# Kernel tuning notes

Measured on AMD Instinct MI355X. Metric: run time of the kernel, lower is better.

## Reference

```python
import jax, jax.numpy as jnp
import numpy as np

B, S, N, C, OUT = 16, 1024, 4096, 768, 256


def setup_inputs() -> dict:
    key = jax.random.key(0)
    k0, k1, k2, k3, k4 = jax.random.split(key, 5)
    seed_xyz = jax.random.normal(k0, (B, S, 3), jnp.float32)   # normalized seed coords
    p_last = jax.random.normal(k1, (B, N, 3), jnp.float32)     # lift3d last-stage coords
    f_last = jax.random.normal(k2, (B, C, N), jnp.float32)     # lift3d last-stage features (channel-first)
    W = jax.random.normal(k3, (OUT, C), jnp.float32) * 0.02    # Conv1d(C, 256, kernel_size=1) weight
    b = jax.random.normal(k4, (OUT,), jnp.float32) * 0.02      # Conv1d bias
    return {"seed_xyz": seed_xyz, "p_last": p_last, "f_last": f_last, "W": W, "b": b}


def reference(seed_xyz, p_last, f_last, W, b):
    # Squared pairwise distances [B,S,N] (argmin invariant to sqrt)
    d2 = (jnp.sum(seed_xyz * seed_xyz, axis=-1, keepdims=True)          # [B,S,1]
          - 2.0 * jnp.einsum('bsd,bnd->bsn', seed_xyz, p_last)          # [B,S,N]
          + jnp.sum(p_last * p_last, axis=-1)[:, None, :])              # [B,1,N]
    idx = jnp.argmin(d2, axis=-1)                                       # [B,S]
    # Gather nearest-neighbor features: [B,C,N] -> [B,C,S]
    gathered = jnp.take_along_axis(f_last, idx[:, None, :], axis=2)
    # 1x1 Conv1d projector: [B,C,S] x [OUT,C] -> [B,OUT,S]
    seed_features = jnp.einsum('bcs,oc->bos', gathered, W) + b[None, :, None]
    return seed_features
```

## Files before the change

kernel.cpp:

```cpp
#include <hip/hip_runtime.h>
#include <stdint.h>

#define B_   16
#define S_   1024
#define N_   4096
#define C_   768
#define OUT_ 256

typedef short bf16x8 __attribute__((ext_vector_type(8)));
typedef short bf16x4 __attribute__((ext_vector_type(4)));
typedef float f32x4  __attribute__((ext_vector_type(4)));

#define GLOBAL_AS __attribute__((address_space(1)))
#define LDS_AS    __attribute__((address_space(3)))

__device__ __forceinline__ unsigned short f2bf(float f) {
    unsigned int u = __float_as_uint(f);
    u += 0x7fffu + ((u >> 16) & 1u);
    return (unsigned short)(u >> 16);
}

__device__ __forceinline__ void gl_lds16(const void* gsrc, void* ldst) {
    __builtin_amdgcn_global_load_lds((const GLOBAL_AS void*)gsrc,
                                     (LDS_AS void*)ldst, 16, 0, 0);
}

__global__ __launch_bounds__(256) void k_wconv(const float* __restrict__ W,
                                               unsigned short* __restrict__ Wb) {
    int i = blockIdx.x * 256 + threadIdx.x;
    Wb[i] = f2bf(W[i]);
}

__global__ __launch_bounds__(256) void k_argmin(const float* __restrict__ seed,
                                                const float* __restrict__ pl,
                                                int* __restrict__ idx_out) {
    const int t    = threadIdx.x;
    const int lane = t & 63;
    const int w    = t >> 6;
    const int gw   = blockIdx.x * 4 + w;
    const int b    = gw >> 8;
    const int s0   = (gw & 255) * 4;

    float sx[4], sy[4], sz[4], s2[4], best[4];
    int   bidx[4];
#pragma unroll
    for (int j = 0; j < 4; ++j) {
        const float* sp = seed + (size_t)(b * S_ + s0 + j) * 3;
        sx[j] = sp[0]; sy[j] = sp[1]; sz[j] = sp[2];
        s2[j] = __fadd_rn(__fadd_rn(__fmul_rn(sx[j], sx[j]),
                                    __fmul_rn(sy[j], sy[j])),
                          __fmul_rn(sz[j], sz[j]));
        best[j] = 3.4e38f;
        bidx[j] = 0;
    }
    const float* pb = pl + (size_t)b * N_ * 3;

    for (int k = 0; k < N_ / 64; ++k) {
        const int   n  = k * 64 + lane;
        const float px = pb[n * 3 + 0];
        const float py = pb[n * 3 + 1];
        const float pz = pb[n * 3 + 2];
        const float p2 = __fadd_rn(__fadd_rn(__fmul_rn(px, px),
                                             __fmul_rn(py, py)),
                                   __fmul_rn(pz, pz));
#pragma unroll
        for (int j = 0; j < 4; ++j) {
            float dot = __fadd_rn(__fadd_rn(__fmul_rn(sx[j], px),
                                            __fmul_rn(sy[j], py)),
                                  __fmul_rn(sz[j], pz));
            float d2  = __fadd_rn(__fsub_rn(s2[j], __fmul_rn(2.0f, dot)), p2);
            if (d2 < best[j]) { best[j] = d2; bidx[j] = n; }
        }
    }

#pragma unroll
    for (int j = 0; j < 4; ++j) {
#pragma unroll
        for (int off = 32; off >= 1; off >>= 1) {
            float ob = __shfl_xor(best[j], off, 64);
            int   oi = __shfl_xor(bidx[j], off, 64);
            bool take = (ob < best[j]) || (ob == best[j] && oi < bidx[j]);
            if (take) { best[j] = ob; bidx[j] = oi; }
        }
        if (lane == 0) idx_out[b * S_ + s0 + j] = bidx[j];
    }
}

__global__ __launch_bounds__(256, 2) void k_pgemm(const float* __restrict__ f,
                                                  const unsigned short* __restrict__ Wb,
                                                  unsigned short* __restrict__ P) {
    __shared__ unsigned short ldsF[128 * 36];
    __shared__ unsigned short ldsW[256 * 32];
    const int t    = threadIdx.x;
    const int b    = blockIdx.x >> 5;
    const int nt   = blockIdx.x & 31;
    const int n0   = nt * 128;
    const int lane = t & 63;
    const int w    = t >> 6;
    const int wm   = w & 1;
    const int wo   = w >> 1;
    const int quad = lane >> 4, l16 = lane & 15;

    f32x4 acc[4][8];
#pragma unroll
    for (int i = 0; i < 4; ++i)
#pragma unroll
        for (int j = 0; j < 8; ++j) acc[i][j] = (f32x4){0.f, 0.f, 0.f, 0.f};

    const int cb = t >> 5;
    const int nb = t & 31;
    const float* fB = f + (size_t)b * C_ * N_ + n0 + nb * 4;
    const unsigned short* wSrc = Wb + (size_t)(t >> 2) * C_ + (t & 3) * 8;

    for (int kt = 0; kt < C_ / 32; ++kt) {
        const int k0 = kt * 32;
#pragma unroll
        for (int i = 0; i < 4; ++i)
            gl_lds16(wSrc + (size_t)i * 64 * C_ + k0, ldsW + i * 2048 + t * 8);
        f32x4 v[4];
#pragma unroll
        for (int j = 0; j < 4; ++j)
            v[j] = *(const f32x4*)(fB + (size_t)(k0 + cb * 4 + j) * N_);
#pragma unroll
        for (int i = 0; i < 4; ++i) {
            bf16x4 pk = {(short)f2bf(v[0][i]), (short)f2bf(v[1][i]),
                         (short)f2bf(v[2][i]), (short)f2bf(v[3][i])};
            *(bf16x4*)(ldsF + (nb * 4 + i) * 36 + cb * 4) = pk;
        }
        __syncthreads();

        bf16x8 aF[4], bF[8];
#pragma unroll
        for (int mi = 0; mi < 4; ++mi) {
            const unsigned short* p = ldsF + (wm * 64 + mi * 16 + l16) * 36 + quad * 8;
            bf16x4 lo = *(const bf16x4*)p;
            bf16x4 hi = *(const bf16x4*)(p + 4);
            aF[mi] = __builtin_shufflevector(lo, hi, 0, 1, 2, 3, 4, 5, 6, 7);
        }
#pragma unroll
        for (int oi = 0; oi < 8; ++oi)
            bF[oi] = *(const bf16x8*)(ldsW + (wo * 128 + oi * 16 + l16) * 32 + quad * 8);
#pragma unroll
        for (int mi = 0; mi < 4; ++mi)
#pragma unroll
            for (int oi = 0; oi < 8; ++oi)
                acc[mi][oi] = __builtin_amdgcn_mfma_f32_16x16x32_bf16(
                    aF[mi], bF[oi], acc[mi][oi], 0, 0, 0);
        __syncthreads();
    }

    unsigned short* Pb = P + ((size_t)b * N_ + n0) * OUT_;
#pragma unroll
    for (int mi = 0; mi < 4; ++mi) {
#pragma unroll
        for (int r = 0; r < 4; ++r) {
            const int n = wm * 64 + mi * 16 + quad * 4 + r;
            unsigned short* row = Pb + (size_t)n * OUT_;
#pragma unroll
            for (int oi = 0; oi < 8; ++oi) {
                const int o = wo * 128 + oi * 16 + l16;
                row[o] = f2bf(acc[mi][oi][r]);
            }
        }
    }
}

__global__ __launch_bounds__(256) void k_out(const unsigned short* __restrict__ P,
                                             const int* __restrict__ idx,
                                             const float* __restrict__ bias,
                                             float* __restrict__ out) {
    __shared__ unsigned short tl[64 * 260];
    const int t  = threadIdx.x;
    const int b  = blockIdx.x >> 4;
    const int st = blockIdx.x & 15;
    const int s0 = st * 64;
    const unsigned short* Pb = P + (size_t)b * N_ * OUT_;

#pragma unroll
    for (int i = 0; i < 8; ++i) {
        const int g = i * 256 + t;
        const int s = g >> 5;
        const int p = g & 31;
        const int n = idx[b * S_ + s0 + s];
        const unsigned short* src = Pb + (size_t)n * OUT_ + p * 8;
        uint2 u0 = *(const uint2*)src;
        uint2 u1 = *(const uint2*)(src + 4);
        *(uint2*)(tl + s * 260 + p * 8)     = u0;
        *(uint2*)(tl + s * 260 + p * 8 + 4) = u1;
    }
    __syncthreads();

    const int lane = t & 63;
    const int w    = t >> 6;
    float* ob = out + (size_t)b * OUT_ * S_ + s0;
#pragma unroll 4
    for (int oo = 0; oo < 64; ++oo) {
        const int o = w * 64 + oo;
        const unsigned short u = tl[lane * 260 + o];
        const float val = __uint_as_float(((unsigned int)u) << 16) + bias[o];
        ob[(size_t)o * S_ + lane] = val;
    }
}

extern "C" void kernel_launch(void* const* d_in, const int* in_sizes, int n_in,
                              void* d_out, int out_size, void* d_ws, size_t ws_size,
                              hipStream_t stream) {
    const float* seed = (const float*)d_in[0];
    const float* pl   = (const float*)d_in[1];
    const float* f    = (const float*)d_in[2];
    const float* W    = (const float*)d_in[3];
    const float* bias = (const float*)d_in[4];
    float* out = (float*)d_out;

    int* idx            = (int*)d_ws;
    unsigned short* Wb  = (unsigned short*)((char*)d_ws + 65536);
    unsigned short* P   = (unsigned short*)((char*)d_ws + 524288);

    k_wconv <<<768,  256, 0, stream>>>(W, Wb);
    k_argmin<<<1024, 256, 0, stream>>>(seed, pl, idx);
    k_pgemm <<<512,  256, 0, stream>>>(f, Wb, P);
    k_out   <<<256,  256, 0, stream>>>(P, idx, bias, out);
}
```

Before: 320.9 us.

## Fuse argmin into projector GEMM kernel and double-buffer GEMM LDS tiles

Merges the nearest-neighbour argmin and the feature projection GEMM into one launch. Every third block runs argmin over 16 seeds per wave, and the other blocks run the GEMM, so the ALU-bound search can overlap with the memory-bound GEMM on the same device. The GEMM loop now double-buffers its LDS tiles: the next K-slice is loaded while MFMAs run on the current one. The cost is twice the LDS per block, more registers in the argmin path (16 seeds per wave), and fewer argmin blocks, each doing more work, which could leave argmin blocks as stragglers.

```diff
diff --git a/kernel.cpp b/kernel.cpp
--- a/kernel.cpp
+++ b/kernel.cpp
@@ -31,70 +31,72 @@
     Wb[i] = f2bf(W[i]);
 }
 
-__global__ __launch_bounds__(256) void k_argmin(const float* __restrict__ seed,
-                                                const float* __restrict__ pl,
-                                                int* __restrict__ idx_out) {
-    const int t    = threadIdx.x;
-    const int lane = t & 63;
-    const int w    = t >> 6;
-    const int gw   = blockIdx.x * 4 + w;
-    const int b    = gw >> 8;
-    const int s0   = (gw & 255) * 4;
-
-    float sx[4], sy[4], sz[4], s2[4], best[4];
-    int   bidx[4];
-#pragma unroll
-    for (int j = 0; j < 4; ++j) {
-        const float* sp = seed + (size_t)(b * S_ + s0 + j) * 3;
-        sx[j] = sp[0]; sy[j] = sp[1]; sz[j] = sp[2];
-        s2[j] = __fadd_rn(__fadd_rn(__fmul_rn(sx[j], sx[j]),
-                                    __fmul_rn(sy[j], sy[j])),
-                          __fmul_rn(sz[j], sz[j]));
-        best[j] = 3.4e38f;
-        bidx[j] = 0;
-    }
-    const float* pb = pl + (size_t)b * N_ * 3;
-
-    for (int k = 0; k < N_ / 64; ++k) {
-        const int   n  = k * 64 + lane;
-        const float px = pb[n * 3 + 0];
-        const float py = pb[n * 3 + 1];
-        const float pz = pb[n * 3 + 2];
-        const float p2 = __fadd_rn(__fadd_rn(__fmul_rn(px, px),
-                                             __fmul_rn(py, py)),
-                                   __fmul_rn(pz, pz));
-#pragma unroll
-        for (int j = 0; j < 4; ++j) {
-            float dot = __fadd_rn(__fadd_rn(__fmul_rn(sx[j], px),
-                                            __fmul_rn(sy[j], py)),
-                                  __fmul_rn(sz[j], pz));
-            float d2  = __fadd_rn(__fsub_rn(s2[j], __fmul_rn(2.0f, dot)), p2);
-            if (d2 < best[j]) { best[j] = d2; bidx[j] = n; }
-        }
-    }
-
-#pragma unroll
-    for (int j = 0; j < 4; ++j) {
-#pragma unroll
-        for (int off = 32; off >= 1; off >>= 1) {
-            float ob = __shfl_xor(best[j], off, 64);
-            int   oi = __shfl_xor(bidx[j], off, 64);
-            bool take = (ob < best[j]) || (ob == best[j] && oi < bidx[j]);
-            if (take) { best[j] = ob; bidx[j] = oi; }
-        }
-        if (lane == 0) idx_out[b * S_ + s0 + j] = bidx[j];
-    }
-}
-
-__global__ __launch_bounds__(256, 2) void k_pgemm(const float* __restrict__ f,
+__global__ __launch_bounds__(256, 2) void k_fused(const float* __restrict__ f,
                                                   const unsigned short* __restrict__ Wb,
-                                                  unsigned short* __restrict__ P) {
-    __shared__ unsigned short ldsF[128 * 36];
-    __shared__ unsigned short ldsW[256 * 32];
-    const int t    = threadIdx.x;
-    const int b    = blockIdx.x >> 5;
-    const int nt   = blockIdx.x & 31;
-    const int n0   = nt * 128;
+                                                  const float* __restrict__ seed,
+                                                  const float* __restrict__ pl,
+                                                  unsigned short* __restrict__ P,
+                                                  int* __restrict__ idx_out) {
+    __shared__ unsigned short ldsF[2][128 * 36];
+    __shared__ unsigned short ldsW[2][256 * 32];
+    const int t   = threadIdx.x;
+    const int bid = blockIdx.x;
+    const int q   = bid / 3;
+    const int r   = bid - q * 3;
+
+    if (r == 2) {
+        const int lane = t & 63;
+        const int w    = t >> 6;
+        const int b    = q >> 4;
+        const int s0   = (q & 15) * 64 + w * 16;
+
+        float sx[16], sy[16], sz[16], s2[16], best[16];
+        int   bidx[16];
+#pragma unroll
+        for (int j = 0; j < 16; ++j) {
+            const float* sp = seed + (size_t)(b * S_ + s0 + j) * 3;
+            sx[j] = sp[0]; sy[j] = sp[1]; sz[j] = sp[2];
+            s2[j] = __fadd_rn(__fadd_rn(__fmul_rn(sx[j], sx[j]),
+                                        __fmul_rn(sy[j], sy[j])),
+                              __fmul_rn(sz[j], sz[j]));
+            best[j] = 3.4e38f;
+            bidx[j] = 0;
+        }
+        const float* pb = pl + (size_t)b * N_ * 3;
+        for (int k = 0; k < N_ / 64; ++k) {
+            const int   n  = k * 64 + lane;
+            const float px = pb[n * 3 + 0];
+            const float py = pb[n * 3 + 1];
+            const float pz = pb[n * 3 + 2];
+            const float p2 = __fadd_rn(__fadd_rn(__fmul_rn(px, px),
+                                                 __fmul_rn(py, py)),
+                                       __fmul_rn(pz, pz));
+#pragma unroll
+            for (int j = 0; j < 16; ++j) {
+                float dot = __fadd_rn(__fadd_rn(__fmul_rn(sx[j], px),
+                                                __fmul_rn(sy[j], py)),
+                                      __fmul_rn(sz[j], pz));
+                float d2  = __fadd_rn(__fsub_rn(s2[j], __fmul_rn(2.0f, dot)), p2);
+                if (d2 < best[j]) { best[j] = d2; bidx[j] = n; }
+            }
+        }
+#pragma unroll
+        for (int j = 0; j < 16; ++j) {
+#pragma unroll
+            for (int off = 32; off >= 1; off >>= 1) {
+                float ob = __shfl_xor(best[j], off, 64);
+                int   oi = __shfl_xor(bidx[j], off, 64);
+                bool take = (ob < best[j]) || (ob == best[j] && oi < bidx[j]);
+                if (take) { best[j] = ob; bidx[j] = oi; }
+            }
+            if (lane == 0) idx_out[b * S_ + s0 + j] = bidx[j];
+        }
+        return;
+    }
+
+    const int pid  = q * 2 + r;
+    const int b    = pid >> 5;
+    const int n0   = (pid & 31) * 128;
     const int lane = t & 63;
     const int w    = t >> 6;
     const int wm   = w & 1;
@@ -112,40 +114,60 @@
     const float* fB = f + (size_t)b * C_ * N_ + n0 + nb * 4;
     const unsigned short* wSrc = Wb + (size_t)(t >> 2) * C_ + (t & 3) * 8;
 
-    for (int kt = 0; kt < C_ / 32; ++kt) {
-        const int k0 = kt * 32;
-#pragma unroll
-        for (int i = 0; i < 4; ++i)
-            gl_lds16(wSrc + (size_t)i * 64 * C_ + k0, ldsW + i * 2048 + t * 8);
-        f32x4 v[4];
-#pragma unroll
-        for (int j = 0; j < 4; ++j)
-            v[j] = *(const f32x4*)(fB + (size_t)(k0 + cb * 4 + j) * N_);
-#pragma unroll
-        for (int i = 0; i < 4; ++i) {
-            bf16x4 pk = {(short)f2bf(v[0][i]), (short)f2bf(v[1][i]),
-                         (short)f2bf(v[2][i]), (short)f2bf(v[3][i])};
-            *(bf16x4*)(ldsF + (nb * 4 + i) * 36 + cb * 4) = pk;
-        }
-        __syncthreads();
+    f32x4 v[4];
+#pragma unroll
+    for (int i = 0; i < 4; ++i)
+        gl_lds16(wSrc + (size_t)i * 64 * C_, &ldsW[0][i * 2048 + t * 8]);
+#pragma unroll
+    for (int j = 0; j < 4; ++j)
+        v[j] = *(const f32x4*)(fB + (size_t)(cb * 4 + j) * N_);
+#pragma unroll
+    for (int i = 0; i < 4; ++i) {
+        bf16x4 pk = {(short)f2bf(v[0][i]), (short)f2bf(v[1][i]),
+                     (short)f2bf(v[2][i]), (short)f2bf(v[3][i])};
+        *(bf16x4*)&ldsF[0][(nb * 4 + i) * 36 + cb * 4] = pk;
+    }
+    __syncthreads();
+
+    for (int kt = 0; kt < 24; ++kt) {
+        const int cur = kt & 1, nxt = cur ^ 1;
+        const bool pre = (kt + 1 < 24);
+        if (pre) {
+            const int k0 = (kt + 1) * 32;
+#pragma unroll
+            for (int i = 0; i < 4; ++i)
+                gl_lds16(wSrc + (size_t)i * 64 * C_ + k0, &ldsW[nxt][i * 2048 + t * 8]);
+#pragma unroll
+            for (int j = 0; j < 4; ++j)
+                v[j] = *(const f32x4*)(fB + (size_t)(k0 + cb * 4 + j) * N_);
+        }
 
         bf16x8 aF[4], bF[8];
 #pragma unroll
         for (int mi = 0; mi < 4; ++mi) {
-            const unsigned short* p = ldsF + (wm * 64 + mi * 16 + l16) * 36 + quad * 8;
+            const unsigned short* p = &ldsF[cur][(wm * 64 + mi * 16 + l16) * 36 + quad * 8];
             bf16x4 lo = *(const bf16x4*)p;
             bf16x4 hi = *(const bf16x4*)(p + 4);
             aF[mi] = __builtin_shufflevector(lo, hi, 0, 1, 2, 3, 4, 5, 6, 7);
         }
 #pragma unroll
         for (int oi = 0; oi < 8; ++oi)
-            bF[oi] = *(const bf16x8*)(ldsW + (wo * 128 + oi * 16 + l16) * 32 + quad * 8);
+            bF[oi] = *(const bf16x8*)&ldsW[cur][(wo * 128 + oi * 16 + l16) * 32 + quad * 8];
 #pragma unroll
         for (int mi = 0; mi < 4; ++mi)
 #pragma unroll
             for (int oi = 0; oi < 8; ++oi)
                 acc[mi][oi] = __builtin_amdgcn_mfma_f32_16x16x32_bf16(
                     aF[mi], bF[oi], acc[mi][oi], 0, 0, 0);
+
+        if (pre) {
+#pragma unroll
+            for (int i = 0; i < 4; ++i) {
+                bf16x4 pk = {(short)f2bf(v[0][i]), (short)f2bf(v[1][i]),
+                             (short)f2bf(v[2][i]), (short)f2bf(v[3][i])};
+                *(bf16x4*)&ldsF[nxt][(nb * 4 + i) * 36 + cb * 4] = pk;
+            }
+        }
         __syncthreads();
     }
 
@@ -153,13 +175,13 @@
 #pragma unroll
     for (int mi = 0; mi < 4; ++mi) {
 #pragma unroll
-        for (int r = 0; r < 4; ++r) {
-            const int n = wm * 64 + mi * 16 + quad * 4 + r;
+        for (int rr = 0; rr < 4; ++rr) {
+            const int n = wm * 64 + mi * 16 + quad * 4 + rr;
             unsigned short* row = Pb + (size_t)n * OUT_;
 #pragma unroll
             for (int oi = 0; oi < 8; ++oi) {
                 const int o = wo * 128 + oi * 16 + l16;
-                row[o] = f2bf(acc[mi][oi][r]);
+                row[o] = f2bf(acc[mi][oi][rr]);
             }
         }
     }
@@ -216,8 +238,7 @@
     unsigned short* Wb  = (unsigned short*)((char*)d_ws + 65536);
     unsigned short* P   = (unsigned short*)((char*)d_ws + 524288);
 
-    k_wconv <<<768,  256, 0, stream>>>(W, Wb);
-    k_argmin<<<1024, 256, 0, stream>>>(seed, pl, idx);
-    k_pgemm <<<512,  256, 0, stream>>>(f, Wb, P);
-    k_out   <<<256,  256, 0, stream>>>(P, idx, bias, out);
-}
+    k_wconv<<<768, 256, 0, stream>>>(W, Wb);
+    k_fused<<<768, 256, 0, stream>>>(f, Wb, seed, pl, P, idx);
+    k_out  <<<256, 256, 0, stream>>>(P, idx, bias, out);
+}
```

Measured after the change: 331.8 us. +3.4%, slower.
